# Optimization experiments

Measured on AMD Instinct MI355X. Metric: run time of the kernel, lower is better.

Reference implementation:

```python
import math
import jax, jax.numpy as jnp
import numpy as np

# ---- static configuration (matches init_kwargs) ----
BATCH, F_IN, F_OUT = 8, 64, 128
B_IN, B_OUT = 32, 16
NL = B_OUT                    # spherical degrees l = 0..NL-1
MDIM = 2 * NL - 1             # dense order axis, m in [-(NL-1), NL-1]
N_BETA_G, N_ALPHA_G = 4, 8
MAX_BETA = math.pi / 8
N_GRID = N_BETA_G * N_ALPHA_G
SCALING = 1.0 / math.sqrt(N_GRID * F_IN * B_OUT ** 4.0 / B_IN ** 2.0)

_LF = np.concatenate([[0.0], np.cumsum(np.log(np.arange(1, 200, dtype=np.float64)))])  # log n!

def _wigner_d(l, betas):
    """Wigner small-d d^l_{m1,m2}(beta) -> [len(betas), 2l+1, 2l+1]."""
    m1 = np.arange(-l, l + 1).reshape(-1, 1, 1)
    m2 = np.arange(-l, l + 1).reshape(1, -1, 1)
    k = np.arange(0, 2 * l + 1).reshape(1, 1, -1)
    a1, a3, a4 = l + m2 - k, m1 - m2 + k, l - m1 - k
    valid = (a1 >= 0) & (a3 >= 0) & (a4 >= 0)
    logc = (0.5 * (_LF[l + m1] + _LF[l - m1] + _LF[l + m2] + _LF[l - m2])
            - _LF[np.clip(a1, 0, None)] - _LF[k]
            - _LF[np.clip(a3, 0, None)] - _LF[np.clip(a4, 0, None)])
    coef = np.where(valid, ((-1.0) ** (m1 - m2 + k)) * np.exp(logc), 0.0)
    c = np.cos(betas / 2.0)[:, None, None, None]
    s = np.sin(betas / 2.0)[:, None, None, None]
    ce = np.clip(2 * l + m2 - m1 - 2 * k, 0, None)
    se = np.clip(m1 - m2 + 2 * k, 0, None)
    return (coef[None] * (c ** ce) * (s ** se)).sum(-1)

# SOFT beta sampling grids
_betas_in = np.pi * (2 * np.arange(2 * B_IN) + 0.5) / (4 * B_IN)
_betas_out = np.pi * (2 * np.arange(2 * B_OUT) + 0.5) / (4 * B_OUT)

# Driscoll-Healy quadrature weights on the input beta grid (alpha measure 2pi/(2b) folded in)
_kk = np.arange(B_IN)
_w = ((2.0 * np.pi / (2 * B_IN)) * (2.0 / B_IN) * np.sin(_betas_in)
      * (np.sin(_betas_in[:, None] * (2 * _kk + 1)) / (2 * _kk + 1)).sum(1))

# kernel grid: s2_near_identity_grid(max_beta=pi/8, n_alpha=8, n_beta=4), beta-major order
_gb = MAX_BETA * np.arange(1, N_BETA_G + 1) / N_BETA_G
_ga = 2 * np.pi * np.arange(N_ALPHA_G) / N_ALPHA_G
GRID_BETA, GRID_ALPHA = [a.ravel() for a in np.meshgrid(_gb, _ga, indexing='ij')]

# W_ANA[beta_j, l, m]  = w_j * d^l_{m,0}(beta_j)            (S2 analysis)
# D_SYN[l, beta_k, m, n] = (2l+1) * d^l_{m,n}(beta_k)       (SO3 synthesis)
# FK[g, l, m]          = d^l_{m,0}(beta_g) * e^{i m alpha_g} (kernel real-FT, s2_rft)
W_ANA = np.zeros((2 * B_IN, NL, MDIM), np.float32)
D_SYN = np.zeros((NL, 2 * B_OUT, MDIM, MDIM), np.float32)
FK = np.zeros((N_GRID, NL, MDIM), np.complex64)
for l in range(NL):
    sl = slice(NL - 1 - l, NL + l)  # dense slots for m = -l..l
    W_ANA[:, l, sl] = (_w[:, None] * _wigner_d(l, _betas_in)[:, :, l]).astype(np.float32)
    D_SYN[l, :, sl, sl] = ((2 * l + 1) * _wigner_d(l, _betas_out)).astype(np.float32)
    m = np.arange(-l, l + 1)
    FK[:, l, sl] = (_wigner_d(l, GRID_BETA)[:, :, l]
                    * np.exp(1j * m[None, :] * GRID_ALPHA[:, None])).astype(np.complex64)
W_ANA, D_SYN, FK = jnp.asarray(W_ANA), jnp.asarray(D_SYN), jnp.asarray(FK)

_M_VALS = np.arange(-(NL - 1), NL)
_BINS_IN = _M_VALS % (2 * B_IN)  # fft bins of the alpha-frequencies m=-15..15


def setup_inputs() -> dict:
    key = jax.random.key(0)
    k1, k2 = jax.random.split(key)
    x = jax.random.normal(k1, (BATCH, F_IN, 2 * B_IN, 2 * B_IN), jnp.float32)
    kernel = jax.random.uniform(k2, (F_IN, F_OUT, N_GRID), jnp.float32, -1.0, 1.0)
    bias = jnp.zeros((1, F_OUT, 1, 1, 1), jnp.float32)
    return {"x": x, "kernel": kernel, "bias": bias}


def _s2_conv(x, kernel, bias):
    # ---- S2 FFT of the input: [B,Fin,2b_in(beta),2b_in(alpha)] -> spectrum [l,m,B,Fin] ----
    xf = jnp.fft.fft(x, axis=-1)              # e^{-i m alpha}
    xm = xf[..., _BINS_IN]                    # [B, Fin, 2b_in, MDIM]
    xhat = jnp.einsum('jlm,bfjm->lmbf', W_ANA, xm)            # [NL, MDIM, B, Fin] complex

    # ---- kernel spherical-harmonic expansion (s2_rft) ----
    kh = jnp.einsum('iog,glm->lmio', (kernel * SCALING).astype(jnp.complex64), FK)

    # ---- per-degree block matmul (s2_mm): z^l_{mn} = sum_i xhat^l_m[i] conj(kh^l_n[i]) ----
    z = jnp.einsum('lmbi,lnio->lmnbo', xhat, jnp.conj(kh))    # [NL, MDIM, MDIM, B, Fout]

    # ---- inverse SO(3) FFT: sum over degrees with (2l+1) d^l_{mn}(beta), then ifft2 over (alpha,gamma) ----
    fmn = jnp.einsum('lkmn,lmnbo->bokmn', D_SYN, z)           # [B, Fout, 2b_out, MDIM, MDIM]
    g = jnp.zeros((BATCH, F_OUT, 2 * B_OUT, 2 * B_OUT, 2 * B_OUT), fmn.dtype)
    g = g.at[..., :MDIM, :MDIM].set(fmn)
    g = jnp.roll(g, shift=(-(NL - 1), -(NL - 1)), axis=(-2, -1))  # m=0 at fft bin 0
    out = jnp.fft.ifft2(g, axes=(-2, -1)).real * float((2 * B_OUT) ** 2)  # e^{+i m alpha}
    return out.astype(jnp.float32) + bias


def reference(x, kernel, bias):
    return _s2_conv(x, kernel, bias)
```

## Files before the change

### kernel.cpp

```cpp
#include <hip/hip_runtime.h>
#include <stdint.h>
#include <math.h>


#define PI_D 3.14159265358979323846
#define SCALING_F 0.002762135864009951f

#define OFF_WANA 0
#define OFF_FKR  31744
#define OFF_FKI  47616
#define OFF_D3   63488
#define OFF_XHAT 317440
#define OFF_WT   317440
#define OFF_KHC  825344
#define OFF_Z2   3053568
#define OFF_T    11180032

typedef unsigned short u16t;
typedef __attribute__((ext_vector_type(8))) short s8v;
typedef __attribute__((ext_vector_type(8))) _Float16 h8v;
typedef __attribute__((ext_vector_type(4))) float f4v;

union frg { uint4 u; uint32_t w[4]; s8v s; h8v h; };

__device__ inline double ipow_d(double x, int e){
  double r = 1.0;
  while (e > 0){ if (e & 1) r *= x; x *= x; e >>= 1; }
  return r;
}

__device__ double wig_d(int l, int m1, int m2, double beta, const double* LF){
  double c = cos(0.5*beta), s = sin(0.5*beta);
  double sum = 0.0;
  for (int k = 0; k <= 2*l; ++k){
    int a1 = l + m2 - k, a3 = m1 - m2 + k, a4 = l - m1 - k;
    if (a1 < 0 || a3 < 0 || a4 < 0) continue;
    double logc = 0.5*(LF[l+m1]+LF[l-m1]+LF[l+m2]+LF[l-m2]) - LF[a1] - LF[k] - LF[a3] - LF[a4];
    double t = exp(logc) * ipow_d(c, a1 + a4) * ipow_d(s, a3 + k);
    sum += (a3 & 1) ? -t : t;
  }
  return sum;
}

__device__ inline uint32_t f2bf(float f){
  uint32_t u = __float_as_uint(f);
  return (u + 0x7fffu + ((u >> 16) & 1u)) >> 16;
}
__device__ inline float bf2f(uint32_t h){ return __uint_as_float((h & 0xffffu) << 16); }
__device__ inline float bf2f_lo(uint32_t h){ return __uint_as_float(h << 16); }
__device__ inline float bf2f_hi(uint32_t h){ return __uint_as_float(h & 0xffff0000u); }
__device__ inline uint32_t pack2(float a, float b){ return f2bf(a) | (f2bf(b) << 16); }

#define LF_INIT \
  __shared__ double LF[40]; \
  if (threadIdx.x == 0){ LF[0] = 0.0; double acc_ = 0.0; for (int n_ = 1; n_ < 40; ++n_){ acc_ += log((double)n_); LF[n_] = acc_; } } \
  __syncthreads();

__global__ void k_zero(float* __restrict__ ws){
  int id = blockIdx.x*256 + threadIdx.x;
  *reinterpret_cast<float4*>(ws + OFF_D3 + (size_t)id*4) = make_float4(0.f,0.f,0.f,0.f);
}

__global__ void k_consts(float* __restrict__ ws){
  LF_INIT
  int bid = blockIdx.x, tid = threadIdx.x;
  if (bid < 124){
    int id = bid*256 + tid;
    if (id >= 31744) return;
    int m = id % 31, l = (id / 31) & 15, j = id / 496;
    int mp = m - 15, amp = mp < 0 ? -mp : mp;
    float val = 0.f;
    if (amp <= l){
      double beta = PI_D*(2*j + 0.5)/128.0;
      double wsum = 0.0;
      for (int kk = 0; kk < 32; ++kk) wsum += sin(beta*(2*kk+1))/(double)(2*kk+1);
      double w = (2.0*PI_D/64.0)*(2.0/32.0)*sin(beta)*wsum;
      val = (float)(w * wig_d(l, mp, 0, beta, LF));
    }
    ws[OFF_WANA + id] = val;
  } else if (bid < 186){
    int id = (bid - 124)*256 + tid;
    if (id >= 15872) return;
    int n = id % 31, l = (id / 31) & 15, g = id / 496;
    int np = n - 15, anp = np < 0 ? -np : np;
    float vr = 0.f, vi = 0.f;
    if (anp <= l){
      double beta = PI_D*((double)((g >> 3) + 1))/32.0;
      double alpha = (PI_D/4.0)*(double)(g & 7);
      double d = wig_d(l, np, 0, beta, LF);
      vr = (float)(d*cos(np*alpha));
      vi = (float)(d*sin(np*alpha));
    }
    ws[OFF_FKR + id] = vr;
    ws[OFF_FKI + id] = vi;
  } else if (bid < 698){
    int bb = bid - 186;
    int k = bb >> 4, l = bb & 15;
    int n21 = 2*l + 1, items = (l+1)*n21;
    double beta = PI_D*(2*k + 0.5)/64.0;
    float fl = (float)(2*l + 1);
    u16t* d3b = reinterpret_cast<u16t*>(ws + OFF_D3);
    for (int item = tid; item < items; item += 256){
      int im = item / n21, in = item - (item/n21)*n21;
      int mn = im*31 + in - l + 15;
      float v = fl * (float)wig_d(l, im, in - l, beta, LF);
      uint32_t hb = f2bf(v);
      uint32_t lb = f2bf(v - bf2f(hb));
      d3b[(mn*32 + k)*32 + l]      = (u16t)hb;
      d3b[(mn*32 + k)*32 + 16 + l] = (u16t)lb;
    }
  } else {
    u16t* wt = reinterpret_cast<u16t*>(ws + OFF_WT);
    for (int idx = tid; idx < 4096; idx += 256){
      int kidx = idx & 31, cc = (idx >> 5) & 15, h = (idx >> 9) & 1;
      int p = (idx >> 10) & 1, nt = (idx >> 11) & 1;
      int q = kidx & 1, nloc = kidx >> 1, n = h*16 + nloc, cg = nt*16 + cc;
      float val = 0.f;
      if (n <= 30){
        double th = 2.0*PI_D*(double)(((17 + n)*cg) & 31)/32.0;
        float wr = (float)cos(th), wi = (float)sin(th);
        val = p ? (q ? wr : wi) : (q ? -wi : wr);
      }
      union { _Float16 hh[2]; u16t us[2]; } cv;
      cv.hh[0] = (_Float16)val; cv.hh[1] = (_Float16)0.f;
      wt[idx] = cv.us[0];
    }
  }
}

__global__ void k_xhat(const float* __restrict__ x, float* __restrict__ ws){
  __shared__ float xl[4096];
  __shared__ float c64[64], s64[64];
  __shared__ float xmr[1024], xmi[1024];
  int tid = threadIdx.x;
  int b = blockIdx.x >> 6, i = blockIdx.x & 63;
  const float* xp = x + (b*64 + i)*4096;
  for (int idx = tid; idx < 4096; idx += 256) xl[idx] = xp[idx];
  if (tid < 64){ double a = 2.0*PI_D*tid/64.0; c64[tid] = (float)cos(a); s64[tid] = (float)sin(a); }
  __syncthreads();
  for (int item = tid; item < 1024; item += 256){
    int j = item >> 4, mi = item & 15;
    float re = 0.f, im = 0.f;
    const float* xr = xl + j*64;
    for (int a = 0; a < 64; ++a){
      int p = (mi*a) & 63;
      re += xr[a]*c64[p];
      im -= xr[a]*s64[p];
    }
    xmr[item] = re; xmi[item] = im;
  }
  __syncthreads();
  {
    int l = tid >> 4, mi = tid & 15;
    if (mi <= l){
      float rr = 0.f, ri = 0.f;
      for (int j = 0; j < 64; ++j){
        float w = ws[OFF_WANA + j*496 + l*31 + 15 + mi];
        rr += w * xmr[j*16 + mi];
        ri += w * xmi[j*16 + mi];
      }
      int dst = OFF_XHAT + ((l*31 + 15 + mi)*8 + b)*128 + i*2;
      ws[dst] = rr; ws[dst+1] = ri;
    }
  }
}

__global__ void k_khc(const float* __restrict__ kern, float* __restrict__ ws){
  __shared__ float kl2[32*66];
  __shared__ float fr[992], fi[992];
  int tid = threadIdx.x;
  int o = blockIdx.x >> 4, l = blockIdx.x & 15;
  for (int idx = tid; idx < 2048; idx += 256){
    int i = idx >> 5, g = idx & 31;
    kl2[g*66 + i] = kern[(i*128 + o)*32 + g];
  }
  for (int idx = tid; idx < 992; idx += 256){
    int g = idx / 31, n = idx - (idx/31)*31;
    fr[idx] = ws[OFF_FKR + g*496 + l*31 + n];
    fi[idx] = ws[OFF_FKI + g*496 + l*31 + n];
  }
  __syncthreads();
  uint32_t* khb = reinterpret_cast<uint32_t*>(ws + OFF_KHC);
  int c1 = (l*(l+1)) >> 1;
  int ntask = (l+1)*32;
  for (int t = tid; t < ntask; t += 256){
    int np = t >> 5, ip = t & 31, i0 = 2*ip;
    float ar0=0.f, ai0=0.f, ar1=0.f, ai1=0.f;
    for (int g = 0; g < 32; ++g){
      float2 kv = *reinterpret_cast<const float2*>(kl2 + g*66 + i0);
      float fv = fr[g*31 + 15 + np], gv = fi[g*31 + 15 + np];
      ar0 += kv.x*fv; ai0 -= kv.x*gv;
      ar1 += kv.y*fv; ai1 -= kv.y*gv;
    }
    size_t base = (size_t)((c1 + np)*128 + o)*64 + i0;
    khb[base]     = pack2(SCALING_F*ar0, SCALING_F*ai0);
    khb[base + 1] = pack2(SCALING_F*ar1, SCALING_F*ai1);
  }
}

__global__ __launch_bounds__(256) void k_zm(float* __restrict__ ws){
  __shared__ uint32_t lds_a[1024];
  __shared__ uint32_t lds_b[8192];
  int tid = threadIdx.x, lane = tid & 63, wv = tid >> 6;
  int c = lane & 15, g = lane >> 4;
  int bid = blockIdx.x;
  int b = bid / 136, t = bid - b*136;
  int l = (int)((sqrtf(8.f*(float)t + 1.f) - 1.f)*0.5f);
  while ((l+1)*(l+2)/2 <= t) ++l;
  while (l*(l+1)/2 > t) --l;
  int np = t - l*(l+1)/2;

  for (int idx = tid; idx < 1024; idx += 256){
    int m = idx >> 6, i = idx & 63;
    uint32_t v = 0u;
    if (m <= l){
      const float* xp = ws + OFF_XHAT + (((l*31 + 15 + m)*8 + b)*128 + 2*i);
      float2 xv = *reinterpret_cast<const float2*>(xp);
      v = pack2(xv.x, xv.y);
    }
    lds_a[(m*64 + i) ^ ((m & 7) << 2)] = v;
  }
  {
    const uint32_t* khb = reinterpret_cast<const uint32_t*>(ws + OFF_KHC);
    size_t rowbase = (size_t)((l*(l+1))/2 + np)*128;
    for (int idx4 = tid; idx4 < 2048; idx4 += 256){
      int o = idx4 >> 4, i4 = idx4 & 15;
      uint4 v = *reinterpret_cast<const uint4*>(khb + (rowbase + o)*64 + i4*4);
      *reinterpret_cast<uint4*>(lds_b + ((o*64 + i4*4) ^ ((o & 7) << 2))) = v;
    }
  }
  __syncthreads();

  frg af[4];
  #pragma unroll
  for (int tt = 0; tt < 4; ++tt)
    af[tt].u = *reinterpret_cast<const uint4*>(lds_a + ((c*64 + tt*16 + g*4) ^ ((c & 7) << 2)));

  uint32_t* z3 = reinterpret_cast<uint32_t*>(ws) + OFF_T;
  int rpos = l*l + l + np, rneg = l*l + l - np;
  for (int ot = wv; ot < 8; ot += 4){
    f4v arp = {0.f,0.f,0.f,0.f}, aip = {0.f,0.f,0.f,0.f};
    f4v arn = {0.f,0.f,0.f,0.f}, ain = {0.f,0.f,0.f,0.f};
    int oc = ot*16 + c;
    #pragma unroll
    for (int tt = 0; tt < 4; ++tt){
      frg bw;
      bw.u = *reinterpret_cast<const uint4*>(lds_b + ((oc*64 + tt*16 + g*4) ^ ((oc & 7) << 2)));
      frg brp, bip;
      #pragma unroll
      for (int j = 0; j < 4; ++j){
        uint32_t w = bw.w[j];
        uint32_t sw = (w >> 16) | (w << 16);
        brp.w[j] = w ^ 0x80000000u;
        bip.w[j] = sw;
      }
      arp = __builtin_amdgcn_mfma_f32_16x16x32_bf16(af[tt].s, brp.s, arp, 0, 0, 0);
      aip = __builtin_amdgcn_mfma_f32_16x16x32_bf16(af[tt].s, bip.s, aip, 0, 0, 0);
      if (np){
        frg brn, bin;
        #pragma unroll
        for (int j = 0; j < 4; ++j){
          uint32_t w = bw.w[j];
          uint32_t sw = (w >> 16) | (w << 16);
          if (np & 1){ brn.w[j] = w ^ 0x80008000u; bin.w[j] = sw ^ 0x80000000u; }
          else       { brn.w[j] = w;               bin.w[j] = sw ^ 0x00008000u; }
        }
        arn = __builtin_amdgcn_mfma_f32_16x16x32_bf16(af[tt].s, brn.s, arn, 0, 0, 0);
        ain = __builtin_amdgcn_mfma_f32_16x16x32_bf16(af[tt].s, bin.s, ain, 0, 0, 0);
      }
    }
    #pragma unroll
    for (int rr = 0; rr < 4; ++rr){
      int m = g*4 + rr;
      z3[((size_t)(b*256 + rpos)*16 + m)*128 + oc] = pack2(arp[rr], aip[rr]);
      if (np)
        z3[((size_t)(b*256 + rneg)*16 + m)*128 + oc] = pack2(arn[rr], ain[rr]);
    }
  }
}

__global__ __launch_bounds__(256) void k_tr(float* __restrict__ ws){
  __shared__ uint32_t zl[256*33];
  int tid = threadIdx.x, bid = blockIdx.x;
  int b = bid >> 6, m = (bid >> 2) & 15, h = bid & 3;
  const uint32_t* z3 = reinterpret_cast<const uint32_t*>(ws) + OFF_T;
  for (int idx = tid; idx < 8192; idx += 256){
    int r = idx >> 5, o = idx & 31;
    zl[r*33 + o] = z3[((size_t)(b*256 + r)*16 + m)*128 + h*32 + o];
  }
  __syncthreads();
  u16t* zr = reinterpret_cast<u16t*>(ws + OFF_Z2);
  u16t* zi = zr + 8126464;
  for (int task = tid; task < 992; task += 256){
    int o = task / 31, nd = task - (task/31)*31;
    int ndp = nd - 15, a = ndp < 0 ? -ndp : ndp;
    uint32_t re[8], im[8];
    #pragma unroll
    for (int j = 0; j < 8; ++j){
      uint32_t r0 = 0u, i0 = 0u, r1 = 0u, i1 = 0u;
      int l0 = 2*j, l1 = 2*j + 1;
      if (l0 >= a){ uint32_t v = zl[(l0*l0 + l0 + ndp)*33 + o]; r0 = v & 0xffffu; i0 = v >> 16; }
      if (l1 >= a){ uint32_t v = zl[(l1*l1 + l1 + ndp)*33 + o]; r1 = v & 0xffffu; i1 = v >> 16; }
      re[j] = r0 | (r1 << 16); im[j] = i0 | (i1 << 16);
    }
    size_t base = (size_t)(b*128 + h*32 + o)*7936 + (m*31 + nd)*16;
    *reinterpret_cast<uint4*>(zr + base)     = make_uint4(re[0],re[1],re[2],re[3]);
    *reinterpret_cast<uint4*>(zr + base + 8) = make_uint4(re[4],re[5],re[6],re[7]);
    *reinterpret_cast<uint4*>(zi + base)     = make_uint4(im[0],im[1],im[2],im[3]);
    *reinterpret_cast<uint4*>(zi + base + 8) = make_uint4(im[4],im[5],im[6],im[7]);
  }
}

__global__ __launch_bounds__(512) void k_fmt(float* __restrict__ ws){
  __shared__ uint32_t fmb[16384];
  int tid = threadIdx.x;
  int lane = tid & 63, wv = tid >> 6;
  int c = lane & 15, g = lane >> 4;
  int bt = blockIdx.x >> 4, m = blockIdx.x & 15;
  const u16t* z2r = reinterpret_cast<const u16t*>(ws + OFF_Z2);
  const u16t* z2i = z2r + 8126464;
  const u16t* d3b = reinterpret_cast<const u16t*>(ws + OFF_D3);
  const u16t* wtb = reinterpret_cast<const u16t*>(ws + OFF_WT);
  fmb[31*512 + (tid ^ 16)] = 0u;

  frg wf[2][2][2];
  #pragma unroll
  for (int nt = 0; nt < 2; ++nt)
    #pragma unroll
    for (int p = 0; p < 2; ++p)
      #pragma unroll
      for (int h = 0; h < 2; ++h)
        wf[nt][p][h].u = *reinterpret_cast<const uint4*>(wtb + ((((nt*2+p)*2+h)*16 + c)*32 + g*8));

  {
    int bo = bt*16 + c;
    int l0 = (g & 1)*8;
    int hl16 = (g >> 1)*16;
    #pragma unroll
    for (int t = 0; t < 4; ++t){
      int nd = wv*4 + t;
      if (nd > 30) break;
      int mn = m*31 + nd;
      frg ar, ai;
      ar.u = *reinterpret_cast<const uint4*>(z2r + ((size_t)bo*496 + mn)*16 + l0);
      ai.u = *reinterpret_cast<const uint4*>(z2i + ((size_t)bo*496 + mn)*16 + l0);
      int key = ((nd >> 2) & 1) << 4;
      #pragma unroll
      for (int kh = 0; kh < 2; ++kh){
        frg bf;
        bf.u = *reinterpret_cast<const uint4*>(d3b + ((size_t)mn*32 + kh*16 + c)*32 + hl16 + l0);
        f4v z4 = {0.f, 0.f, 0.f, 0.f};
        f4v cre = __builtin_amdgcn_mfma_f32_16x16x32_bf16(ar.s, bf.s, z4, 0, 0, 0);
        f4v cim = __builtin_amdgcn_mfma_f32_16x16x32_bf16(ai.s, bf.s, z4, 0, 0, 0);
        #pragma unroll
        for (int rr = 0; rr < 4; ++rr){
          int bok = (g*4 + rr)*32 + kh*16 + c;
          union { _Float16 hh[2]; uint32_t u; } pk;
          pk.hh[0] = (_Float16)cre[rr];
          pk.hh[1] = (_Float16)cim[rr];
          fmb[nd*512 + (bok ^ key)] = pk.u;
        }
      }
    }
  }
  __syncthreads();
  uint32_t* tglob = reinterpret_cast<uint32_t*>(ws) + OFF_T;
  #pragma unroll
  for (int q = 0; q < 4; ++q){
    int mt = wv*4 + q;
    int arow = mt*16 + c;
    frg A0, A1;
    #pragma unroll
    for (int j = 0; j < 4; ++j){
      int nd0 = g*4 + j, nd1 = nd0 + 16;
      A0.w[j] = fmb[nd0*512 + (arow ^ (((nd0 >> 2) & 1) << 4))];
      A1.w[j] = fmb[nd1*512 + (arow ^ (((nd1 >> 2) & 1) << 4))];
    }
    #pragma unroll
    for (int nt = 0; nt < 2; ++nt){
      f4v z4 = {0.f, 0.f, 0.f, 0.f};
      f4v tre = __builtin_amdgcn_mfma_f32_16x16x32_f16(A0.h, wf[nt][0][0].h, z4, 0, 0, 0);
      tre     = __builtin_amdgcn_mfma_f32_16x16x32_f16(A1.h, wf[nt][0][1].h, tre, 0, 0, 0);
      f4v tim = __builtin_amdgcn_mfma_f32_16x16x32_f16(A0.h, wf[nt][1][0].h, z4, 0, 0, 0);
      tim     = __builtin_amdgcn_mfma_f32_16x16x32_f16(A1.h, wf[nt][1][1].h, tim, 0, 0, 0);
      #pragma unroll
      for (int rr = 0; rr < 4; ++rr){
        int bokl = mt*16 + g*4 + rr;
        int bokg = (bt*16 + (bokl >> 5))*32 + (bokl & 31);
        tglob[(size_t)(bokg*16 + m)*32 + nt*16 + c] = pack2(tre[rr], tim[rr]);
      }
    }
  }
}

__global__ void k_out(const float* __restrict__ bias, float* __restrict__ out,
                      const float* __restrict__ ws){
  __shared__ uint32_t tl[2048];
  __shared__ float2 tw2[32];
  int tid = threadIdx.x;
  int b4 = blockIdx.x*4;
  const uint32_t* tg = reinterpret_cast<const uint32_t*>(ws) + OFF_T + (size_t)b4*512;
  for (int idx = tid; idx < 2048; idx += 256) tl[idx] = tg[idx];
  if (tid < 32){ double a = 2.0*PI_D*tid/32.0; tw2[tid] = make_float2((float)cos(a), (float)sin(a)); }
  __syncthreads();
  int aq = tid >> 5, c = tid & 31;
  for (int q = 0; q < 4; ++q){
    int bok = b4 + q;
    const uint32_t* tq = tl + q*512;
    float t0r = bf2f(tq[c]);
    float U0=0,U1=0,U2=0,U3=0,V0=0,V1=0,V2=0,V3=0;
    int p = aq;
    #pragma unroll
    for (int m = 1; m < 16; ++m){
      uint32_t wv = tq[m*32 + c];
      float tr = bf2f_lo(wv), ti = bf2f_hi(wv);
      float2 T = tw2[p];
      float u = tr*T.x - ti*T.y;
      float v = tr*T.y + ti*T.x;
      int j = m & 3;
      if      (j == 0){ U0 += u; V0 += v; }
      else if (j == 1){ U1 += u; V1 += v; }
      else if (j == 2){ U2 += u; V2 += v; }
      else            { U3 += u; V3 += v; }
      p = (p + aq) & 31;
    }
    float bia = bias[(bok >> 5) & 127];
    float* op = out + (size_t)bok*1024 + c;
    op[aq*32]      = t0r + 2.f*(U0+U1+U2+U3) + bia;
    op[(aq+8)*32]  = t0r + 2.f*(U0-V1-U2+V3) + bia;
    op[(aq+16)*32] = t0r + 2.f*(U0-U1+U2-U3) + bia;
    op[(aq+24)*32] = t0r + 2.f*(U0+V1-U2-V3) + bia;
  }
}

extern "C" void kernel_launch(void* const* d_in, const int* in_sizes, int n_in,
                              void* d_out, int out_size, void* d_ws, size_t ws_size,
                              hipStream_t stream) {
  const float* x    = (const float*)d_in[0];
  const float* kern = (const float*)d_in[1];
  const float* bias = (const float*)d_in[2];
  float* out = (float*)d_out;
  float* ws  = (float*)d_ws;

  k_zero  <<<dim3(248),  dim3(256), 0, stream>>>(ws);
  k_consts<<<dim3(699),  dim3(256), 0, stream>>>(ws);
  k_xhat  <<<dim3(512),  dim3(256), 0, stream>>>(x, ws);
  k_khc   <<<dim3(2048), dim3(256), 0, stream>>>(kern, ws);
  k_zm    <<<dim3(1088), dim3(256), 0, stream>>>(ws);
  k_tr    <<<dim3(512),  dim3(256), 0, stream>>>(ws);
  k_fmt   <<<dim3(1024), dim3(512), 0, stream>>>(ws);
  k_out   <<<dim3(8192), dim3(256), 0, stream>>>(bias, out, ws);
}
```

Measured before the change: 272.3 us.

## Transpose W_ANA and Z2 layouts for coalesced access, hoist quadrature weights

Stores the analysis weights l,m-major with j contiguous so each thread in the xhat kernel reads a contiguous row. It also computes the per-beta quadrature sum once per block in shared memory instead of once per element. The Z2 intermediate is re-laid out as [mn][b,o][l], so the transpose kernel writes and the fmt kernel reads contiguous 16-element chunks across adjacent (b,o). This changes the access pattern across three kernels and needs producer and consumer to agree on the layout.

Measured after the change: 263.4 us. 1.03x faster.

```diff
diff --git a/kernel.cpp b/kernel.cpp
--- a/kernel.cpp
+++ b/kernel.cpp
@@ -65,19 +65,30 @@
   LF_INIT
   int bid = blockIdx.x, tid = threadIdx.x;
   if (bid < 124){
-    int id = bid*256 + tid;
-    if (id >= 31744) return;
+    __shared__ double wj2[2];
+    int id0 = bid*256;
+    int jbase = id0/496;
+    if (tid < 2){
+      int j = jbase + tid;
+      double wv_ = 0.0;
+      if (j < 64){
+        double beta = PI_D*(2*j + 0.5)/128.0;
+        double wsum = 0.0;
+        for (int kk = 0; kk < 32; ++kk) wsum += sin(beta*(2*kk+1))/(double)(2*kk+1);
+        wv_ = (2.0*PI_D/64.0)*(2.0/32.0)*sin(beta)*wsum;
+      }
+      wj2[tid] = wv_;
+    }
+    __syncthreads();
+    int id = id0 + tid;
     int m = id % 31, l = (id / 31) & 15, j = id / 496;
     int mp = m - 15, amp = mp < 0 ? -mp : mp;
     float val = 0.f;
     if (amp <= l){
       double beta = PI_D*(2*j + 0.5)/128.0;
-      double wsum = 0.0;
-      for (int kk = 0; kk < 32; ++kk) wsum += sin(beta*(2*kk+1))/(double)(2*kk+1);
-      double w = (2.0*PI_D/64.0)*(2.0/32.0)*sin(beta)*wsum;
-      val = (float)(w * wig_d(l, mp, 0, beta, LF));
-    }
-    ws[OFF_WANA + id] = val;
+      val = (float)(wj2[j - jbase] * wig_d(l, mp, 0, beta, LF));
+    }
+    ws[OFF_WANA + (l*31 + m)*64 + j] = val;
   } else if (bid < 186){
     int id = (bid - 124)*256 + tid;
     if (id >= 15872) return;
@@ -154,8 +165,9 @@
     int l = tid >> 4, mi = tid & 15;
     if (mi <= l){
       float rr = 0.f, ri = 0.f;
+      const float* wrow = ws + OFF_WANA + (l*31 + 15 + mi)*64;
       for (int j = 0; j < 64; ++j){
-        float w = ws[OFF_WANA + j*496 + l*31 + 15 + mi];
+        float w = wrow[j];
         rr += w * xmr[j*16 + mi];
         ri += w * xmi[j*16 + mi];
       }
@@ -292,7 +304,7 @@
   u16t* zr = reinterpret_cast<u16t*>(ws + OFF_Z2);
   u16t* zi = zr + 8126464;
   for (int task = tid; task < 992; task += 256){
-    int o = task / 31, nd = task - (task/31)*31;
+    int nd = task >> 5, o = task & 31;
     int ndp = nd - 15, a = ndp < 0 ? -ndp : ndp;
     uint32_t re[8], im[8];
     #pragma unroll
@@ -303,7 +315,7 @@
       if (l1 >= a){ uint32_t v = zl[(l1*l1 + l1 + ndp)*33 + o]; r1 = v & 0xffffu; i1 = v >> 16; }
       re[j] = r0 | (r1 << 16); im[j] = i0 | (i1 << 16);
     }
-    size_t base = (size_t)(b*128 + h*32 + o)*7936 + (m*31 + nd)*16;
+    size_t base = (size_t)(m*31 + nd)*16384 + (size_t)(b*128 + h*32 + o)*16;
     *reinterpret_cast<uint4*>(zr + base)     = make_uint4(re[0],re[1],re[2],re[3]);
     *reinterpret_cast<uint4*>(zr + base + 8) = make_uint4(re[4],re[5],re[6],re[7]);
     *reinterpret_cast<uint4*>(zi + base)     = make_uint4(im[0],im[1],im[2],im[3]);
@@ -333,17 +345,17 @@
         wf[nt][p][h].u = *reinterpret_cast<const uint4*>(wtb + ((((nt*2+p)*2+h)*16 + c)*32 + g*8));
 
   {
-    int bo = bt*16 + c;
     int l0 = (g & 1)*8;
     int hl16 = (g >> 1)*16;
+    size_t bo16 = (size_t)(bt*16 + c)*16;
     #pragma unroll
     for (int t = 0; t < 4; ++t){
       int nd = wv*4 + t;
       if (nd > 30) break;
       int mn = m*31 + nd;
       frg ar, ai;
-      ar.u = *reinterpret_cast<const uint4*>(z2r + ((size_t)bo*496 + mn)*16 + l0);
-      ai.u = *reinterpret_cast<const uint4*>(z2i + ((size_t)bo*496 + mn)*16 + l0);
+      ar.u = *reinterpret_cast<const uint4*>(z2r + (size_t)mn*16384 + bo16 + l0);
+      ai.u = *reinterpret_cast<const uint4*>(z2i + (size_t)mn*16384 + bo16 + l0);
       int key = ((nd >> 2) & 1) << 4;
       #pragma unroll
       for (int kh = 0; kh < 2; ++kh){
```
